# Kernel optimization log

Measured on AMD Instinct MI355X. Metric: run time of the kernel, lower is better.

The kernel has to match this reference:

```python
import jax, jax.numpy as jnp
import numpy as np

B, T_MEL, T_TXT = 16, 2048, 1024
D_MODEL, D_ENC_M, D_ENC_T = 512, 512, 512
LN_EPS = 1e-5


def setup_inputs() -> dict:
    key = jax.random.key(0)
    ks = jax.random.split(key, 9)
    mel_encoding = jax.random.normal(ks[0], (B, T_MEL, D_ENC_M), dtype=jnp.float32)
    text_encoding = jax.random.normal(ks[1], (B, T_TXT, D_ENC_T), dtype=jnp.float32)
    mel_mask = jax.random.randint(ks[2], (B, T_MEL), 0, 2).astype(bool)
    mel_mask = mel_mask.at[:, 0].set(False)  # guarantee >=1 unmasked key per row
    src_mask = jax.random.randint(ks[3], (B, T_TXT), 0, 2).astype(bool)
    # Projection weights stored [in, out] (torch Linear does x @ W.T)
    sc = 1.0 / np.sqrt(D_ENC_M)
    Wq = jax.random.uniform(ks[4], (D_ENC_T, D_MODEL), jnp.float32, -sc, sc)
    Wk = jax.random.uniform(ks[5], (D_ENC_M, D_MODEL), jnp.float32, -sc, sc)
    Wv = jax.random.uniform(ks[6], (D_ENC_M, D_MODEL), jnp.float32, -sc, sc)
    ln_gamma = jnp.ones((D_MODEL,), jnp.float32)
    ln_beta = jnp.zeros((D_MODEL,), jnp.float32)
    return {"mel_encoding": mel_encoding, "text_encoding": text_encoding,
            "mel_mask": mel_mask, "src_mask": src_mask,
            "Wq": Wq, "Wk": Wk, "Wv": Wv,
            "ln_gamma": ln_gamma, "ln_beta": ln_beta}


def reference(mel_encoding, text_encoding, mel_mask, src_mask, Wq, Wk, Wv, ln_gamma, ln_beta):
    temperature = jnp.sqrt(jnp.float32(D_ENC_M))
    q = jnp.einsum('btd,dm->btm', text_encoding, Wq)   # [B, T_txt, d_model]
    k = jnp.einsum('bsd,dm->bsm', mel_encoding, Wk)    # [B, T_mel, d_model]
    v = jnp.einsum('bsd,dm->bsm', mel_encoding, Wv)
    # attn_mask = outer product of src_mask and mel_mask (True -> masked)
    attn_mask = src_mask[:, :, None] & mel_mask[:, None, :]  # [B, T_txt, T_mel]
    scores = jnp.einsum('btm,bsm->bts', q, k) / temperature
    scores = jnp.where(attn_mask, -jnp.inf, scores)
    attn = jax.nn.softmax(scores, axis=2)
    output = jnp.einsum('bts,bsm->btm', attn, v)
    # dropout is identity at inference; LayerNorm over last dim
    mean = jnp.mean(output, axis=-1, keepdims=True)
    var = jnp.var(output, axis=-1, keepdims=True)
    output = (output - mean) * jax.lax.rsqrt(var + LN_EPS) * ln_gamma + ln_beta
    return output, attn
```

## Files before the change

### kernel.cpp

```cpp
#include <hip/hip_runtime.h>

#define DEV __device__ __forceinline__

typedef __attribute__((ext_vector_type(8))) short short8v;
typedef __attribute__((ext_vector_type(4))) float f32x4;

DEV unsigned short f2bf(float f) {
  unsigned int x = __float_as_uint(f);
  x = x + 0x7FFFu + ((x >> 16) & 1u);
  return (unsigned short)(x >> 16);
}
DEV float bf2f(unsigned short u) {
  return __uint_as_float(((unsigned)u) << 16);
}

DEV int swz_byte(int row, int kElem) {
  int chunk = ((kElem >> 3) ^ (row & 7));
  return row * 128 + (chunk << 4) + ((kElem & 7) << 1);
}

template <int ROUNDS>
DEV void stage(const unsigned short* __restrict__ g, int ld,
               unsigned short* tile, int tid) {
  const int wave = tid >> 6, l = tid & 63;
#pragma unroll
  for (int p = 0; p < ROUNDS; ++p) {
    const int r = (p << 5) + (wave << 3) + (l >> 3);
    const int c = ((l & 7) ^ (r & 7)) << 3;
    const unsigned short* src = g + (long)r * ld + c;
#if __has_builtin(__builtin_amdgcn_global_load_lds)
    unsigned short* dst = tile + (p << 11) + (wave << 9);
    __builtin_amdgcn_global_load_lds(
        (const __attribute__((address_space(1))) void*)src,
        (__attribute__((address_space(3))) void*)dst, 16, 0, 0);
#else
    short8v v = *reinterpret_cast<const short8v*>(src);
    *reinterpret_cast<short8v*>(reinterpret_cast<char*>(tile) +
                                (p << 12) + (wave << 10) + (l << 4)) = v;
#endif
  }
}

template <int BM>
DEV void stage_f32(const float* __restrict__ g, int ld,
                   unsigned short* tile, int tid) {
  const int rl = tid >> 4;
  const int c4 = (tid & 15) << 2;
#pragma unroll
  for (int p = 0; p < BM / 16; ++p) {
    const int row = (p << 4) + rl;
    const float4 f = *reinterpret_cast<const float4*>(g + (long)row * ld + c4);
    ushort4 pack;
    pack.x = f2bf(f.x); pack.y = f2bf(f.y); pack.z = f2bf(f.z); pack.w = f2bf(f.w);
    *reinterpret_cast<ushort4*>(reinterpret_cast<char*>(tile) +
                                swz_byte(row, c4)) = pack;
  }
}

template <int BM, int EPI, int GM, bool AF32>
__global__ __launch_bounds__(256) void gemm_bf16(
    const void* __restrict__ Av, const unsigned short* __restrict__ B,
    void* __restrict__ Cout, int M, int N, int K,
    long aBatch, long bBatch, long cBatch,
    const int* __restrict__ srcMask, const int* __restrict__ melMask,
    float scale, float* __restrict__ stats) {
  constexpr int NI = BM / 32;
  __shared__ unsigned short As[BM * 64];
  __shared__ unsigned short Bs[128 * 64];
  const int tid = threadIdx.x;
  const int lane = tid & 63;
  const int wave = tid >> 6;
  int z, bmi, bni;
  if constexpr (GM == 1) {
    const int id = blockIdx.x;
    z = (id & 7) | ((id >> 10) << 3);
    const int ib = (id >> 3) & 127;
    bni = ib & 15;
    bmi = ib >> 4;
  } else if constexpr (GM == 2) {
    bmi = blockIdx.x; bni = blockIdx.y; z = blockIdx.z;
  } else {
    bni = blockIdx.x; bmi = blockIdx.y; z = blockIdx.z;
  }
  const int bm = bmi * BM;
  const int bn = bni * 128;
  const unsigned short* Bb = B + (long)z * bBatch;
  const long cOff = (long)z * cBatch;
  const int wr = (wave >> 1) * (BM / 2);
  const int wc = (wave & 1) * 64;
  const int l15 = lane & 15;
  const int lHi = lane >> 4;

  f32x4 acc[NI][4] = {};

  for (int kt = 0; kt < K; kt += 64) {
    if constexpr (AF32) {
      stage_f32<BM>((const float*)Av + (long)z * aBatch + (long)bm * K + kt, K, As, tid);
    } else {
      stage<BM / 32>((const unsigned short*)Av + (long)z * aBatch + (long)bm * K + kt,
                     K, As, tid);
    }
    stage<4>(Bb + (long)bn * K + kt, K, Bs, tid);
    __syncthreads();
#pragma unroll
    for (int ks = 0; ks < 2; ++ks) {
      const int k0 = (ks << 5) + (lHi << 3);
      short8v af[NI], bfr[4];
#pragma unroll
      for (int i = 0; i < NI; ++i)
        af[i] = *reinterpret_cast<const short8v*>(
            reinterpret_cast<const char*>(As) + swz_byte(wr + i * 16 + l15, k0));
#pragma unroll
      for (int j = 0; j < 4; ++j)
        bfr[j] = *reinterpret_cast<const short8v*>(
            reinterpret_cast<const char*>(Bs) + swz_byte(wc + j * 16 + l15, k0));
#pragma unroll
      for (int i = 0; i < NI; ++i)
#pragma unroll
        for (int j = 0; j < 4; ++j)
          acc[i][j] = __builtin_amdgcn_mfma_f32_16x16x32_bf16(af[i], bfr[j], acc[i][j], 0, 0, 0);
    }
    __syncthreads();
  }

  if constexpr (EPI == 2) {
    __shared__ float redM[128][2];
    __shared__ float redS[128][2];
    const int wcIdx = wave & 1;
#pragma unroll
    for (int i = 0; i < NI; ++i) {
#pragma unroll
      for (int rr = 0; rr < 4; ++rr) {
        const int rloc = wr + i * 16 + lHi * 4 + rr;
        const int rb = bm + rloc;
        const bool sm = srcMask[z * 1024 + rb] != 0;
        float vals[4];
        float m_l = -3.0e38f;
#pragma unroll
        for (int j = 0; j < 4; ++j) {
          const int c = bn + wc + j * 16 + l15;
          const bool mm = melMask[z * 2048 + c] != 0;
          const float vf = (sm && mm) ? -1e30f : acc[i][j][rr] * scale;
          vals[j] = vf;
          reinterpret_cast<unsigned short*>(Cout)[cOff + (long)rb * N + c] = f2bf(vf);
          m_l = fmaxf(m_l, vf);
        }
#pragma unroll
        for (int o = 1; o < 16; o <<= 1) m_l = fmaxf(m_l, __shfl_xor(m_l, o, 64));
        float s_l = 0.f;
#pragma unroll
        for (int j = 0; j < 4; ++j) s_l += __expf(vals[j] - m_l);
#pragma unroll
        for (int o = 1; o < 16; o <<= 1) s_l += __shfl_xor(s_l, o, 64);
        if (l15 == 0) { redM[rloc][wcIdx] = m_l; redS[rloc][wcIdx] = s_l; }
      }
    }
    __syncthreads();
    if (tid < 128) {
      const float m0 = redM[tid][0], m1 = redM[tid][1];
      const float Mx = fmaxf(m0, m1);
      const float S = redS[tid][0] * __expf(m0 - Mx) + redS[tid][1] * __expf(m1 - Mx);
      const long sidx = ((long)(z * 1024 + bm + tid)) * 32 + (long)bni * 2;
      stats[sidx] = Mx;
      stats[sidx + 1] = S;
    }
  } else {
#pragma unroll
    for (int i = 0; i < NI; ++i) {
#pragma unroll
      for (int j = 0; j < 4; ++j) {
        const int rb = bm + wr + i * 16 + lHi * 4;
        const int c = bn + wc + j * 16 + l15;
#pragma unroll
        for (int r = 0; r < 4; ++r) {
          const float v = acc[i][j][r];
          const long idx = cOff + (long)(rb + r) * N + c;
          if constexpr (EPI == 0)
            reinterpret_cast<unsigned short*>(Cout)[idx] = f2bf(v);
          else
            reinterpret_cast<float*>(Cout)[idx] = v;
        }
      }
    }
  }
}

__global__ __launch_bounds__(256) void pv_smx(
    const unsigned short* __restrict__ sbf, const unsigned short* __restrict__ vT,
    float* __restrict__ attn, float* __restrict__ out,
    const float* __restrict__ stats) {
  __shared__ unsigned short As[32 * 64];
  __shared__ unsigned short Bs[128 * 64];
  __shared__ float rowM[32], rowInv[32];
  const int id = blockIdx.x;
  const int z = (id & 7) | ((id >> 10) << 3);
  const int ib = (id >> 3) & 127;
  const int mt = ib & 31, nt = ib >> 5;
  const int bm = mt * 32, bn = nt * 128;
  const int tid = threadIdx.x, lane = tid & 63, wave = tid >> 6;

  if (tid < 32) {
    const float* st = stats + ((long)(z * 1024 + bm + tid)) * 32;
    float Mx = -3.0e38f;
#pragma unroll
    for (int t = 0; t < 16; ++t) Mx = fmaxf(Mx, st[t * 2]);
    float S = 0.f;
#pragma unroll
    for (int t = 0; t < 16; ++t) S += st[t * 2 + 1] * __expf(st[t * 2] - Mx);
    rowM[tid] = Mx;
    rowInv[tid] = 1.0f / S;
  }
  __syncthreads();

  const int ar = tid >> 3;
  const int ac = (tid & 7) << 3;
  const float mR = rowM[ar];
  const float invR = rowInv[ar];
  const long aOff = ((long)z * 1024 + bm + ar) * 2048 + ac;
  const unsigned short* vTb = vT + ((long)z * 512 + bn) * 2048;
  const int wr = (wave >> 1) * 16, wc = (wave & 1) * 64;
  const int l15 = lane & 15, lHi = lane >> 4;

  f32x4 acc[4] = {};

  for (int kt = 0; kt < 2048; kt += 64) {
    stage<4>(vTb + kt, 2048, Bs, tid);
    const short8v s0 = *reinterpret_cast<const short8v*>(sbf + aOff + kt);
    float e[8];
#pragma unroll
    for (int u = 0; u < 8; ++u)
      e[u] = __expf(bf2f((unsigned short)s0[u]) - mR) * invR;
    if ((kt >> 9) == nt) {
      float* ap = attn + aOff + kt;
      float4 w0, w1;
      w0.x = e[0]; w0.y = e[1]; w0.z = e[2]; w0.w = e[3];
      w1.x = e[4]; w1.y = e[5]; w1.z = e[6]; w1.w = e[7];
      *reinterpret_cast<float4*>(ap) = w0;
      *reinterpret_cast<float4*>(ap + 4) = w1;
    }
    short8v pk;
#pragma unroll
    for (int u = 0; u < 8; ++u) pk[u] = (short)f2bf(e[u]);
    *reinterpret_cast<short8v*>(reinterpret_cast<char*>(As) + swz_byte(ar, ac)) = pk;
    __syncthreads();

#pragma unroll
    for (int ks = 0; ks < 2; ++ks) {
      const int k0 = (ks << 5) + (lHi << 3);
      short8v af, bfr[4];
      af = *reinterpret_cast<const short8v*>(
          reinterpret_cast<const char*>(As) + swz_byte(wr + l15, k0));
#pragma unroll
      for (int j = 0; j < 4; ++j)
        bfr[j] = *reinterpret_cast<const short8v*>(
            reinterpret_cast<const char*>(Bs) + swz_byte(wc + j * 16 + l15, k0));
#pragma unroll
      for (int j = 0; j < 4; ++j)
        acc[j] = __builtin_amdgcn_mfma_f32_16x16x32_bf16(af, bfr[j], acc[j], 0, 0, 0);
    }
    __syncthreads();
  }

#pragma unroll
  for (int j = 0; j < 4; ++j) {
    const int row = bm + wr + lHi * 4;
    const int col = bn + wc + j * 16 + l15;
#pragma unroll
    for (int rr = 0; rr < 4; ++rr)
      out[((long)z * 1024 + row + rr) * 512 + col] = acc[j][rr];
  }
}

__global__ __launch_bounds__(256) void f32_to_bf16(
    const float* __restrict__ in, unsigned short* __restrict__ out, long n) {
  long i = ((long)blockIdx.x * blockDim.x + threadIdx.x) * 8;
  const long stride = (long)gridDim.x * blockDim.x * 8;
  for (; i < n; i += stride) {
    const float4 a = *reinterpret_cast<const float4*>(in + i);
    const float4 b = *reinterpret_cast<const float4*>(in + i + 4);
    short8v o;
    o[0] = (short)f2bf(a.x); o[1] = (short)f2bf(a.y);
    o[2] = (short)f2bf(a.z); o[3] = (short)f2bf(a.w);
    o[4] = (short)f2bf(b.x); o[5] = (short)f2bf(b.y);
    o[6] = (short)f2bf(b.z); o[7] = (short)f2bf(b.w);
    *reinterpret_cast<short8v*>(out + i) = o;
  }
}

__global__ __launch_bounds__(256) void conv_w2(
    const float* __restrict__ Wq, const float* __restrict__ Wk,
    unsigned short* __restrict__ wqbf, unsigned short* __restrict__ wkbf) {
  const float* in = blockIdx.y ? Wk : Wq;
  unsigned short* out = blockIdx.y ? wkbf : wqbf;
  const long i = ((long)blockIdx.x * 256 + threadIdx.x) * 8;
  const float4 a = *reinterpret_cast<const float4*>(in + i);
  const float4 b = *reinterpret_cast<const float4*>(in + i + 4);
  short8v o;
  o[0] = (short)f2bf(a.x); o[1] = (short)f2bf(a.y);
  o[2] = (short)f2bf(a.z); o[3] = (short)f2bf(a.w);
  o[4] = (short)f2bf(b.x); o[5] = (short)f2bf(b.y);
  o[6] = (short)f2bf(b.z); o[7] = (short)f2bf(b.w);
  *reinterpret_cast<short8v*>(out + i) = o;
}

__global__ __launch_bounds__(256) void transpose_wv(
    const float* __restrict__ Wv, unsigned short* __restrict__ WvT) {
  __shared__ float t[32][33];
  const int bx = blockIdx.x * 32;
  const int by = blockIdx.y * 32;
  const int tx = threadIdx.x, ty = threadIdx.y;
#pragma unroll
  for (int i = 0; i < 4; ++i)
    t[ty + i * 8][tx] = Wv[(long)(by + ty + i * 8) * 512 + bx + tx];
  __syncthreads();
#pragma unroll
  for (int i = 0; i < 4; ++i)
    WvT[(long)(bx + ty + i * 8) * 512 + by + tx] = f2bf(t[tx][ty + i * 8]);
}

__global__ __launch_bounds__(64) void layernorm_rows(
    float* __restrict__ out, const float* __restrict__ gamma, const float* __restrict__ beta) {
  const long row = blockIdx.x;
  float4* p = reinterpret_cast<float4*>(out + row * 512);
  const int lane = threadIdx.x;
  float4 a = p[lane];
  float4 b = p[lane + 64];
  float s = ((a.x + a.y) + (a.z + a.w)) + ((b.x + b.y) + (b.z + b.w));
  float s2 = ((a.x * a.x + a.y * a.y) + (a.z * a.z + a.w * a.w)) +
             ((b.x * b.x + b.y * b.y) + (b.z * b.z + b.w * b.w));
#pragma unroll
  for (int o = 32; o; o >>= 1) {
    s += __shfl_xor(s, o, 64);
    s2 += __shfl_xor(s2, o, 64);
  }
  const float mean = s * (1.0f / 512.0f);
  const float var = s2 * (1.0f / 512.0f) - mean * mean;
  const float rstd = rsqrtf(var + 1e-5f);
  const float4 g0 = reinterpret_cast<const float4*>(gamma)[lane];
  const float4 g1 = reinterpret_cast<const float4*>(gamma)[lane + 64];
  const float4 c0 = reinterpret_cast<const float4*>(beta)[lane];
  const float4 c1 = reinterpret_cast<const float4*>(beta)[lane + 64];
  a.x = (a.x - mean) * rstd * g0.x + c0.x;
  a.y = (a.y - mean) * rstd * g0.y + c0.y;
  a.z = (a.z - mean) * rstd * g0.z + c0.z;
  a.w = (a.w - mean) * rstd * g0.w + c0.w;
  b.x = (b.x - mean) * rstd * g1.x + c1.x;
  b.y = (b.y - mean) * rstd * g1.y + c1.y;
  b.z = (b.z - mean) * rstd * g1.z + c1.z;
  b.w = (b.w - mean) * rstd * g1.w + c1.w;
  p[lane] = a;
  p[lane + 64] = b;
}

extern "C" void kernel_launch(void* const* d_in, const int* in_sizes, int n_in,
                              void* d_out, int out_size, void* d_ws, size_t ws_size,
                              hipStream_t stream) {
  const float* mel  = (const float*)d_in[0];
  const float* text = (const float*)d_in[1];
  const int* melMask = (const int*)d_in[2];
  const int* srcMask = (const int*)d_in[3];
  const float* Wq = (const float*)d_in[4];
  const float* Wk = (const float*)d_in[5];
  const float* Wv = (const float*)d_in[6];
  const float* gamma = (const float*)d_in[7];
  const float* beta  = (const float*)d_in[8];

  float* out = (float*)d_out;
  float* attn = (float*)d_out + (long)16 * 1024 * 512;

  unsigned short* ws = (unsigned short*)d_ws;
  unsigned short* wqbf = ws;
  unsigned short* wkbf = wqbf + 512 * 512;
  unsigned short* wvT  = wkbf + 512 * 512;
  unsigned short* Mt   = wvT + 512 * 512;
  unsigned short* melbf = Mt + 512 * 512;
  unsigned short* qbf  = melbf + (long)16 * 2048 * 512;
  unsigned short* vT   = qbf + (long)16 * 1024 * 512;
  unsigned short* sbf  = vT + (long)16 * 512 * 2048;
  float* stats = (float*)(sbf + (long)16 * 1024 * 2048);

  conv_w2<<<dim3(128, 2), 256, 0, stream>>>(Wq, Wk, wqbf, wkbf);
  transpose_wv<<<dim3(16, 16), dim3(32, 8), 0, stream>>>(Wv, wvT);
  f32_to_bf16<<<dim3(4096), 256, 0, stream>>>(mel, melbf, (long)16 * 2048 * 512);

  gemm_bf16<128, 0, 0, false><<<dim3(4, 4, 1), 256, 0, stream>>>(
      wkbf, wqbf, Mt, 512, 512, 512, 0, 0, 0, nullptr, nullptr, 1.0f, nullptr);
  gemm_bf16<128, 0, 2, true><<<dim3(128, 4, 1), 256, 0, stream>>>(
      text, Mt, qbf, 16384, 512, 512, 0, 0, 0, nullptr, nullptr, 1.0f, nullptr);
  gemm_bf16<128, 0, 0, false><<<dim3(16, 4, 16), 256, 0, stream>>>(
      wvT, melbf, vT, 512, 2048, 512, 0, (long)2048 * 512, (long)512 * 2048,
      nullptr, nullptr, 1.0f, nullptr);
  gemm_bf16<128, 2, 1, false><<<dim3(2048), 256, 0, stream>>>(
      qbf, melbf, sbf, 1024, 2048, 512,
      (long)1024 * 512, (long)2048 * 512, (long)1024 * 2048,
      srcMask, melMask, 0.044194173824159216f, stats);
  pv_smx<<<dim3(2048), 256, 0, stream>>>(sbf, vT, attn, out, stats);
  layernorm_rows<<<dim3(16 * 1024), 64, 0, stream>>>(out, gamma, beta);
}
```

Baseline: 267.0 us.

## Split attn-probability write into own kernel and enlarge PV tile to 64 rows

The fp32 attention-probability write moves out of the PV GEMM into a separate row-wise kernel. The PV kernel's M-tile doubles from 32 to 64 rows with 2x4 MFMA accumulators per wave, halving the grid and the number of times V is re-read. The kernel also software-prefetches the next bf16 score chunk into registers. In exchange, the exp/normalize work is done twice (once in each kernel), there is an extra launch, and the scores are read twice.

```diff
diff --git a/kernel.cpp b/kernel.cpp
--- a/kernel.cpp
+++ b/kernel.cpp
@@ -173,33 +173,55 @@
         const int c = bn + wc + j * 16 + l15;
 #pragma unroll
         for (int r = 0; r < 4; ++r) {
-          const float v = acc[i][j][r];
           const long idx = cOff + (long)(rb + r) * N + c;
-          if constexpr (EPI == 0)
-            reinterpret_cast<unsigned short*>(Cout)[idx] = f2bf(v);
-          else
-            reinterpret_cast<float*>(Cout)[idx] = v;
+          reinterpret_cast<unsigned short*>(Cout)[idx] = f2bf(acc[i][j][r]);
         }
       }
     }
   }
 }
 
-__global__ __launch_bounds__(256) void pv_smx(
+__global__ __launch_bounds__(256) void attn_write(
+    const unsigned short* __restrict__ sbf, const float* __restrict__ stats,
+    float* __restrict__ attn) {
+  const long row = blockIdx.x;
+  const float* st = stats + row * 32;
+  float Mx = -3.0e38f;
+#pragma unroll
+  for (int t = 0; t < 16; ++t) Mx = fmaxf(Mx, st[t * 2]);
+  float S = 0.f;
+#pragma unroll
+  for (int t = 0; t < 16; ++t) S += st[t * 2 + 1] * __expf(st[t * 2] - Mx);
+  const float inv = 1.0f / S;
+  const long base = row * 2048 + threadIdx.x * 8;
+  const short8v s = *reinterpret_cast<const short8v*>(sbf + base);
+  float4 w0, w1;
+  w0.x = __expf(bf2f((unsigned short)s[0]) - Mx) * inv;
+  w0.y = __expf(bf2f((unsigned short)s[1]) - Mx) * inv;
+  w0.z = __expf(bf2f((unsigned short)s[2]) - Mx) * inv;
+  w0.w = __expf(bf2f((unsigned short)s[3]) - Mx) * inv;
+  w1.x = __expf(bf2f((unsigned short)s[4]) - Mx) * inv;
+  w1.y = __expf(bf2f((unsigned short)s[5]) - Mx) * inv;
+  w1.z = __expf(bf2f((unsigned short)s[6]) - Mx) * inv;
+  w1.w = __expf(bf2f((unsigned short)s[7]) - Mx) * inv;
+  *reinterpret_cast<float4*>(attn + base) = w0;
+  *reinterpret_cast<float4*>(attn + base + 4) = w1;
+}
+
+__global__ __launch_bounds__(256) void pv(
     const unsigned short* __restrict__ sbf, const unsigned short* __restrict__ vT,
-    float* __restrict__ attn, float* __restrict__ out,
-    const float* __restrict__ stats) {
-  __shared__ unsigned short As[32 * 64];
+    float* __restrict__ out, const float* __restrict__ stats) {
+  __shared__ unsigned short As[64 * 64];
   __shared__ unsigned short Bs[128 * 64];
-  __shared__ float rowM[32], rowInv[32];
+  __shared__ float rowM[64], rowInv[64];
   const int id = blockIdx.x;
-  const int z = (id & 7) | ((id >> 10) << 3);
-  const int ib = (id >> 3) & 127;
-  const int mt = ib & 31, nt = ib >> 5;
-  const int bm = mt * 32, bn = nt * 128;
+  const int z = (id & 7) | ((id >> 9) << 3);
+  const int ib = (id >> 3) & 63;
+  const int mt = ib & 15, nt = ib >> 4;
+  const int bm = mt * 64, bn = nt * 128;
   const int tid = threadIdx.x, lane = tid & 63, wave = tid >> 6;
 
-  if (tid < 32) {
+  if (tid < 64) {
     const float* st = stats + ((long)(z * 1024 + bm + tid)) * 32;
     float Mx = -3.0e38f;
 #pragma unroll
@@ -212,63 +234,66 @@
   }
   __syncthreads();
 
-  const int ar = tid >> 3;
-  const int ac = (tid & 7) << 3;
+  const int ar = tid >> 2;
+  const int ac = (tid & 3) << 4;
   const float mR = rowM[ar];
   const float invR = rowInv[ar];
   const long aOff = ((long)z * 1024 + bm + ar) * 2048 + ac;
   const unsigned short* vTb = vT + ((long)z * 512 + bn) * 2048;
-  const int wr = (wave >> 1) * 16, wc = (wave & 1) * 64;
+  const int wr = (wave >> 1) * 32, wc = (wave & 1) * 64;
   const int l15 = lane & 15, lHi = lane >> 4;
 
-  f32x4 acc[4] = {};
+  f32x4 acc[2][4] = {};
+  short8v s0 = *reinterpret_cast<const short8v*>(sbf + aOff);
+  short8v s1 = *reinterpret_cast<const short8v*>(sbf + aOff + 8);
 
   for (int kt = 0; kt < 2048; kt += 64) {
     stage<4>(vTb + kt, 2048, Bs, tid);
-    const short8v s0 = *reinterpret_cast<const short8v*>(sbf + aOff + kt);
-    float e[8];
-#pragma unroll
-    for (int u = 0; u < 8; ++u)
-      e[u] = __expf(bf2f((unsigned short)s0[u]) - mR) * invR;
-    if ((kt >> 9) == nt) {
-      float* ap = attn + aOff + kt;
-      float4 w0, w1;
-      w0.x = e[0]; w0.y = e[1]; w0.z = e[2]; w0.w = e[3];
-      w1.x = e[4]; w1.y = e[5]; w1.z = e[6]; w1.w = e[7];
-      *reinterpret_cast<float4*>(ap) = w0;
-      *reinterpret_cast<float4*>(ap + 4) = w1;
-    }
-    short8v pk;
-#pragma unroll
-    for (int u = 0; u < 8; ++u) pk[u] = (short)f2bf(e[u]);
-    *reinterpret_cast<short8v*>(reinterpret_cast<char*>(As) + swz_byte(ar, ac)) = pk;
+    short8v pk0, pk1;
+#pragma unroll
+    for (int u = 0; u < 8; ++u) {
+      pk0[u] = (short)f2bf(__expf(bf2f((unsigned short)s0[u]) - mR) * invR);
+      pk1[u] = (short)f2bf(__expf(bf2f((unsigned short)s1[u]) - mR) * invR);
+    }
+    *reinterpret_cast<short8v*>(reinterpret_cast<char*>(As) + swz_byte(ar, ac)) = pk0;
+    *reinterpret_cast<short8v*>(reinterpret_cast<char*>(As) + swz_byte(ar, ac + 8)) = pk1;
+    if (kt < 2048 - 64) {
+      s0 = *reinterpret_cast<const short8v*>(sbf + aOff + kt + 64);
+      s1 = *reinterpret_cast<const short8v*>(sbf + aOff + kt + 72);
+    }
     __syncthreads();
 
 #pragma unroll
     for (int ks = 0; ks < 2; ++ks) {
       const int k0 = (ks << 5) + (lHi << 3);
-      short8v af, bfr[4];
-      af = *reinterpret_cast<const short8v*>(
-          reinterpret_cast<const char*>(As) + swz_byte(wr + l15, k0));
+      short8v af[2], bfr[4];
+#pragma unroll
+      for (int i = 0; i < 2; ++i)
+        af[i] = *reinterpret_cast<const short8v*>(
+            reinterpret_cast<const char*>(As) + swz_byte(wr + i * 16 + l15, k0));
 #pragma unroll
       for (int j = 0; j < 4; ++j)
         bfr[j] = *reinterpret_cast<const short8v*>(
             reinterpret_cast<const char*>(Bs) + swz_byte(wc + j * 16 + l15, k0));
 #pragma unroll
-      for (int j = 0; j < 4; ++j)
-        acc[j] = __builtin_amdgcn_mfma_f32_16x16x32_bf16(af, bfr[j], acc[j], 0, 0, 0);
+      for (int i = 0; i < 2; ++i)
+#pragma unroll
+        for (int j = 0; j < 4; ++j)
+          acc[i][j] = __builtin_amdgcn_mfma_f32_16x16x32_bf16(af[i], bfr[j], acc[i][j], 0, 0, 0);
     }
     __syncthreads();
   }
 
 #pragma unroll
-  for (int j = 0; j < 4; ++j) {
-    const int row = bm + wr + lHi * 4;
-    const int col = bn + wc + j * 16 + l15;
-#pragma unroll
-    for (int rr = 0; rr < 4; ++rr)
-      out[((long)z * 1024 + row + rr) * 512 + col] = acc[j][rr];
-  }
+  for (int i = 0; i < 2; ++i)
+#pragma unroll
+    for (int j = 0; j < 4; ++j) {
+      const int row = bm + wr + i * 16 + lHi * 4;
+      const int col = bn + wc + j * 16 + l15;
+#pragma unroll
+      for (int rr = 0; rr < 4; ++rr)
+        out[((long)z * 1024 + row + rr) * 512 + col] = acc[i][j][rr];
+    }
 }
 
 __global__ __launch_bounds__(256) void f32_to_bf16(
@@ -394,6 +419,7 @@
       qbf, melbf, sbf, 1024, 2048, 512,
       (long)1024 * 512, (long)2048 * 512, (long)1024 * 2048,
       srcMask, melMask, 0.044194173824159216f, stats);
-  pv_smx<<<dim3(2048), 256, 0, stream>>>(sbf, vT, attn, out, stats);
+  attn_write<<<dim3(16 * 1024), 256, 0, stream>>>(sbf, stats, attn);
+  pv<<<dim3(1024), 256, 0, stream>>>(sbf, vT, out, stats);
   layernorm_rows<<<dim3(16 * 1024), 64, 0, stream>>>(out, gamma, beta);
 }
```

Result: slower. 273.2 us (+2.4%).
